# Kernel optimization log

Hardware: AMD Instinct MI355X
Metric: run time of the kernel (lower is better)

## Reference

```python
import jax, jax.numpy as jnp
import numpy as np

B, H, D, E = 64, 8, 64, 512          # batch, heads, head_dim, embed_dim
NB, BS = 32, 128                     # blocks per sequence, block size
L = NB * BS                          # max kv length (4096)
POS = 2048                           # decode position in cache


def setup_inputs() -> dict:
    key = jax.random.key(0)
    ks = jax.random.split(key, 12)
    s = E ** -0.5
    return {
        "hidden_states": jax.random.normal(ks[0], (B, 1, E), jnp.float32),
        "q_w": jax.random.normal(ks[1], (E, E), jnp.float32) * s,
        "q_b": jnp.zeros((E,), jnp.float32),
        "k_w": jax.random.normal(ks[2], (E, E), jnp.float32) * s,
        "k_b": jnp.zeros((E,), jnp.float32),
        "v_w": jax.random.normal(ks[3], (E, E), jnp.float32) * s,
        "v_b": jnp.zeros((E,), jnp.float32),
        "o_w": jax.random.normal(ks[4], (E, E), jnp.float32) * s,
        "o_b": jnp.zeros((E,), jnp.float32),
        "kcache": jax.random.normal(ks[5], (B, H, NB, BS, D), jnp.float32),
        "vcache": jax.random.normal(ks[6], (B, H, NB, BS, D), jnp.float32),
        "attention_mask": jnp.zeros((B, 1, 1, L), jnp.float32),  # additive mask
        "cache_position": POS,
        "block_tables": jax.random.randint(ks[7], (B, NB), 0, NB, jnp.int32),
    }


def reference(hidden_states, q_w, q_b, k_w, k_b, v_w, v_b, o_w, o_b,
              kcache, vcache, attention_mask, cache_position, block_tables):
    scaling = D ** -0.5
    # projections for the single decode token; q is pre-scaled (op gets scale=1.0)
    q = (hidden_states[:, 0] @ q_w.T + q_b).reshape(B, H, D) * scaling
    k_new = (hidden_states[:, 0] @ k_w.T + k_b).reshape(B, H, D)
    v_new = (hidden_states[:, 0] @ v_w.T + v_b).reshape(B, H, D)

    # gather physical blocks per sequence via block table -> [B, NB, H, BS, D]
    bidx = jnp.arange(B)[:, None]
    k_g = kcache[bidx, :, block_tables].transpose(0, 2, 1, 3, 4).reshape(B, H, L, D)
    v_g = vcache[bidx, :, block_tables].transpose(0, 2, 1, 3, 4).reshape(B, H, L, D)

    # write current token's k/v at cache_position (paged cache update)
    k_g = k_g.at[:, :, cache_position, :].set(k_new)
    v_g = v_g.at[:, :, cache_position, :].set(v_new)

    # add-softmax attention: scores = qk + mask
    scores = jnp.einsum('bhd,bhld->bhl', q, k_g) + attention_mask[:, :, 0, :]
    attn = jax.nn.softmax(scores, axis=-1)
    ctx = jnp.einsum('bhl,bhld->bhd', attn, v_g).reshape(B, 1, E)
    return ctx @ o_w.T + o_b
```

## Files before the change

### kernel.cpp

```cpp
#include <hip/hip_runtime.h>
#include <math.h>

#define BB 64
#define HH 8
#define Dh 64
#define EE 512
#define NBLK 32
#define BSZ 128
#define LL 4096

__global__ __launch_bounds__(512) void qkv_proj(
    const float* __restrict__ hidden,
    const float* __restrict__ q_w, const float* __restrict__ q_b,
    const float* __restrict__ k_w, const float* __restrict__ k_b,
    const float* __restrict__ v_w, const float* __restrict__ v_b,
    float* __restrict__ ws)
{
    const int b = blockIdx.x;
    const int proj = blockIdx.y;
    const int e = threadIdx.x;
    __shared__ float sh[EE];
    sh[e] = hidden[b * EE + e];
    __syncthreads();

    const float* w; const float* bias; float* out; float scale;
    if (proj == 0)      { w = q_w; bias = q_b; out = ws;             scale = 0.125f; }
    else if (proj == 1) { w = k_w; bias = k_b; out = ws + BB * EE;   scale = 1.0f; }
    else                { w = v_w; bias = v_b; out = ws + 2*BB*EE;   scale = 1.0f; }

    const float4* wr = (const float4*)(w + (size_t)e * EE);
    const float4* h4 = (const float4*)sh;
    float acc = bias[e];
    #pragma unroll 8
    for (int i = 0; i < EE/4; ++i) {
        float4 a = wr[i]; float4 x = h4[i];
        acc += a.x*x.x + a.y*x.y + a.z*x.z + a.w*x.w;
    }
    out[b * EE + e] = acc * scale;
}

__global__ __launch_bounds__(512) void attn(
    const float* __restrict__ ws,
    const float* __restrict__ kcache, const float* __restrict__ vcache,
    const float* __restrict__ mask,
    const int* __restrict__ cpos_p,
    const int* __restrict__ btab,
    float* __restrict__ ctx)
{
    const int bh = blockIdx.x;
    const int b  = bh >> 3;
    const int tid = threadIdx.x;
    const int grp = tid >> 4;
    const int l16 = tid & 15;
    const int wave = tid >> 6;
    const int lane = tid & 63;

    __shared__ float  s_scores[LL];
    __shared__ float  s_q[Dh];
    __shared__ int    s_bt[NBLK];
    __shared__ float  s_red[8];
    __shared__ float  s_b;
    __shared__ float4 s_vp[8][16];

    const float* qv   = ws;
    const float* knew = ws + BB * EE;
    const float* vnew = ws + 2 * BB * EE;

    if (tid < Dh)   s_q[tid]  = qv[(size_t)bh * Dh + tid];
    if (tid < NBLK) s_bt[tid] = btab[b * NBLK + tid];
    const int cpos = *cpos_p;
    __syncthreads();

    const float4 q4 = ((const float4*)s_q)[l16];
    const size_t base = (size_t)bh * NBLK * BSZ * Dh;
    const float4* knew4 = (const float4*)(knew + (size_t)bh * Dh);
    const float4* vnew4 = (const float4*)(vnew + (size_t)bh * Dh);

    #pragma unroll 4
    for (int step = 0; step < LL/32; ++step) {
        const int row = step * 32 + grp;
        const int nb = row >> 7, j = row & (BSZ - 1);
        const float4* kr = (const float4*)(kcache + base + ((size_t)s_bt[nb] * BSZ + j) * Dh);
        if (row == cpos) kr = knew4;
        float4 kv = kr[l16];
        float p = q4.x*kv.x + q4.y*kv.y + q4.z*kv.z + q4.w*kv.w;
        p += __shfl_xor(p, 1); p += __shfl_xor(p, 2);
        p += __shfl_xor(p, 4); p += __shfl_xor(p, 8);
        if (l16 == 0) s_scores[row] = p;
    }
    __syncthreads();

    float loc[8];
    float m = -3.4e38f;
    const float* mrow = mask + (size_t)b * LL;
    #pragma unroll
    for (int i = 0; i < 8; ++i) {
        const int idx = tid + 512 * i;
        loc[i] = s_scores[idx] + mrow[idx];
        m = fmaxf(m, loc[i]);
    }
    #pragma unroll
    for (int o = 1; o < 64; o <<= 1) m = fmaxf(m, __shfl_xor(m, o));
    if (lane == 0) s_red[wave] = m;
    __syncthreads();
    if (tid == 0) {
        float mm = s_red[0];
        #pragma unroll
        for (int i = 1; i < 8; ++i) mm = fmaxf(mm, s_red[i]);
        s_b = mm;
    }
    __syncthreads();
    m = s_b;

    float ssum = 0.f;
    #pragma unroll
    for (int i = 0; i < 8; ++i) { loc[i] = expf(loc[i] - m); ssum += loc[i]; }
    #pragma unroll
    for (int o = 1; o < 64; o <<= 1) ssum += __shfl_xor(ssum, o);
    __syncthreads();
    if (lane == 0) s_red[wave] = ssum;
    __syncthreads();
    if (tid == 0) {
        float s = 0.f;
        #pragma unroll
        for (int i = 0; i < 8; ++i) s += s_red[i];
        s_b = 1.0f / s;
    }
    __syncthreads();
    const float inv = s_b;
    #pragma unroll
    for (int i = 0; i < 8; ++i) s_scores[tid + 512 * i] = loc[i] * inv;
    __syncthreads();

    float4 acc = make_float4(0.f, 0.f, 0.f, 0.f);
    #pragma unroll 4
    for (int step = 0; step < LL/32; ++step) {
        const int row = step * 32 + grp;
        const int nb = row >> 7, j = row & (BSZ - 1);
        const float4* vr = (const float4*)(vcache + base + ((size_t)s_bt[nb] * BSZ + j) * Dh);
        if (row == cpos) vr = vnew4;
        float4 vv = vr[l16];
        const float w = s_scores[row];
        acc.x += w * vv.x; acc.y += w * vv.y; acc.z += w * vv.z; acc.w += w * vv.w;
    }
    #pragma unroll
    for (int o = 16; o < 64; o <<= 1) {
        acc.x += __shfl_xor(acc.x, o);
        acc.y += __shfl_xor(acc.y, o);
        acc.z += __shfl_xor(acc.z, o);
        acc.w += __shfl_xor(acc.w, o);
    }
    if (lane < 16) s_vp[wave][l16] = acc;
    __syncthreads();
    if (tid < 16) {
        float4 t = s_vp[0][tid];
        #pragma unroll
        for (int w = 1; w < 8; ++w) {
            float4 u = s_vp[w][tid];
            t.x += u.x; t.y += u.y; t.z += u.z; t.w += u.w;
        }
        ((float4*)(ctx + (size_t)bh * Dh))[tid] = t;
    }
}

__global__ __launch_bounds__(512) void out_proj(
    const float* __restrict__ ctx,
    const float* __restrict__ o_w, const float* __restrict__ o_b,
    float* __restrict__ out)
{
    const int b = blockIdx.x;
    const int e = threadIdx.x;
    __shared__ float sh[EE];
    sh[e] = ctx[b * EE + e];
    __syncthreads();
    const float4* wr = (const float4*)(o_w + (size_t)e * EE);
    const float4* h4 = (const float4*)sh;
    float acc = o_b[e];
    #pragma unroll 8
    for (int i = 0; i < EE/4; ++i) {
        float4 a = wr[i]; float4 x = h4[i];
        acc += a.x*x.x + a.y*x.y + a.z*x.z + a.w*x.w;
    }
    out[b * EE + e] = acc;
}

extern "C" void kernel_launch(void* const* d_in, const int* in_sizes, int n_in,
                              void* d_out, int out_size, void* d_ws, size_t ws_size,
                              hipStream_t stream)
{
    const float* hidden = (const float*)d_in[0];
    const float* q_w = (const float*)d_in[1];
    const float* q_b = (const float*)d_in[2];
    const float* k_w = (const float*)d_in[3];
    const float* k_b = (const float*)d_in[4];
    const float* v_w = (const float*)d_in[5];
    const float* v_b = (const float*)d_in[6];
    const float* o_w = (const float*)d_in[7];
    const float* o_b = (const float*)d_in[8];
    const float* kcache = (const float*)d_in[9];
    const float* vcache = (const float*)d_in[10];
    const float* mask = (const float*)d_in[11];
    const int* cpos = (const int*)d_in[12];
    const int* btab = (const int*)d_in[13];

    float* ws  = (float*)d_ws;
    float* ctx = ws + 3 * BB * EE;

    qkv_proj<<<dim3(BB, 3), 512, 0, stream>>>(hidden, q_w, q_b, k_w, k_b, v_w, v_b, ws);
    attn<<<dim3(BB * HH), 512, 0, stream>>>(ws, kcache, vcache, mask, cpos, btab, ctx);
    out_proj<<<dim3(BB), 512, 0, stream>>>(ctx, o_w, o_b, (float*)d_out);
}
```

Baseline: 231.4 us.

## Fuse attention into single-pass online softmax and batch-tile projection GEMVs

The attention kernel now streams K and V together in one pass with an online softmax per 16-lane group, merging the 32 group partials at the end. This removes the 16KB score buffer, the separate max/sum/normalize phases and their barriers, and the second read sweep over the block table. Projection kernels now process 4 batch rows per block and split the output dimension and reduction across threads, so each weight load is reused across batch rows. Loads use nontemporal hints and fast __expf. The online rescaling adds per-row exp work, and the extra grid dimensions change occupancy.

```diff
diff --git a/kernel.cpp b/kernel.cpp
--- a/kernel.cpp
+++ b/kernel.cpp
@@ -8,6 +8,10 @@
 #define NBLK 32
 #define BSZ 128
 #define LL 4096
+#define BG 4
+#define RC 128
+
+typedef float f4 __attribute__((ext_vector_type(4)));
 
 __global__ __launch_bounds__(512) void qkv_proj(
     const float* __restrict__ hidden,
@@ -16,11 +20,16 @@
     const float* __restrict__ v_w, const float* __restrict__ v_b,
     float* __restrict__ ws)
 {
-    const int b = blockIdx.x;
-    const int proj = blockIdx.y;
-    const int e = threadIdx.x;
-    __shared__ float sh[EE];
-    sh[e] = hidden[b * EE + e];
+    const int bg = blockIdx.x, proj = blockIdx.y, chunk = blockIdx.z;
+    const int tid = threadIdx.x;
+    const int r  = tid & (RC - 1);
+    const int l4 = tid >> 7;
+
+    __shared__ float sh[BG][EE];
+    __shared__ float sp[4][BG][RC];
+
+    for (int i = tid; i < BG * EE; i += 512)
+        sh[i >> 9][i & (EE - 1)] = hidden[(bg * BG + (i >> 9)) * EE + (i & (EE - 1))];
     __syncthreads();
 
     const float* w; const float* bias; float* out; float scale;
@@ -28,15 +37,26 @@
     else if (proj == 1) { w = k_w; bias = k_b; out = ws + BB * EE;   scale = 1.0f; }
     else                { w = v_w; bias = v_b; out = ws + 2*BB*EE;   scale = 1.0f; }
 
-    const float4* wr = (const float4*)(w + (size_t)e * EE);
-    const float4* h4 = (const float4*)sh;
-    float acc = bias[e];
+    const int e = chunk * RC + r;
+    const float4* wr = (const float4*)(w + (size_t)e * EE + l4 * 128);
+    float acc[BG] = {0.f, 0.f, 0.f, 0.f};
     #pragma unroll 8
-    for (int i = 0; i < EE/4; ++i) {
-        float4 a = wr[i]; float4 x = h4[i];
-        acc += a.x*x.x + a.y*x.y + a.z*x.z + a.w*x.w;
-    }
-    out[b * EE + e] = acc * scale;
+    for (int i = 0; i < 32; ++i) {
+        const float4 a = wr[i];
+        #pragma unroll
+        for (int b = 0; b < BG; ++b) {
+            const float4 x = ((const float4*)sh[b])[l4 * 32 + i];
+            acc[b] += a.x*x.x + a.y*x.y + a.z*x.z + a.w*x.w;
+        }
+    }
+    #pragma unroll
+    for (int b = 0; b < BG; ++b) sp[l4][b][r] = acc[b];
+    __syncthreads();
+
+    const int b2 = tid >> 7, r2 = tid & (RC - 1);
+    const int e2 = chunk * RC + r2;
+    const float v = sp[0][b2][r2] + sp[1][b2][r2] + sp[2][b2][r2] + sp[3][b2][r2];
+    out[(bg * BG + b2) * EE + e2] = (v + bias[e2]) * scale;
 }
 
 __global__ __launch_bounds__(512) void attn(
@@ -52,15 +72,12 @@
     const int tid = threadIdx.x;
     const int grp = tid >> 4;
     const int l16 = tid & 15;
-    const int wave = tid >> 6;
-    const int lane = tid & 63;
-
-    __shared__ float  s_scores[LL];
+
     __shared__ float  s_q[Dh];
     __shared__ int    s_bt[NBLK];
-    __shared__ float  s_red[8];
-    __shared__ float  s_b;
-    __shared__ float4 s_vp[8][16];
+    __shared__ float  s_m[32];
+    __shared__ float  s_s[32];
+    __shared__ float4 s_acc[32][16];
 
     const float* qv   = ws;
     const float* knew = ws + BB * EE;
@@ -73,92 +90,71 @@
 
     const float4 q4 = ((const float4*)s_q)[l16];
     const size_t base = (size_t)bh * NBLK * BSZ * Dh;
-    const float4* knew4 = (const float4*)(knew + (size_t)bh * Dh);
-    const float4* vnew4 = (const float4*)(vnew + (size_t)bh * Dh);
-
-    #pragma unroll 4
-    for (int step = 0; step < LL/32; ++step) {
-        const int row = step * 32 + grp;
-        const int nb = row >> 7, j = row & (BSZ - 1);
-        const float4* kr = (const float4*)(kcache + base + ((size_t)s_bt[nb] * BSZ + j) * Dh);
-        if (row == cpos) kr = knew4;
-        float4 kv = kr[l16];
-        float p = q4.x*kv.x + q4.y*kv.y + q4.z*kv.z + q4.w*kv.w;
-        p += __shfl_xor(p, 1); p += __shfl_xor(p, 2);
-        p += __shfl_xor(p, 4); p += __shfl_xor(p, 8);
-        if (l16 == 0) s_scores[row] = p;
-    }
-    __syncthreads();
-
-    float loc[8];
-    float m = -3.4e38f;
+    const f4* knew4 = (const f4*)(knew + (size_t)bh * Dh);
+    const f4* vnew4 = (const f4*)(vnew + (size_t)bh * Dh);
     const float* mrow = mask + (size_t)b * LL;
-    #pragma unroll
-    for (int i = 0; i < 8; ++i) {
-        const int idx = tid + 512 * i;
-        loc[i] = s_scores[idx] + mrow[idx];
-        m = fmaxf(m, loc[i]);
-    }
-    #pragma unroll
-    for (int o = 1; o < 64; o <<= 1) m = fmaxf(m, __shfl_xor(m, o));
-    if (lane == 0) s_red[wave] = m;
-    __syncthreads();
-    if (tid == 0) {
-        float mm = s_red[0];
-        #pragma unroll
-        for (int i = 1; i < 8; ++i) mm = fmaxf(mm, s_red[i]);
-        s_b = mm;
-    }
-    __syncthreads();
-    m = s_b;
-
-    float ssum = 0.f;
-    #pragma unroll
-    for (int i = 0; i < 8; ++i) { loc[i] = expf(loc[i] - m); ssum += loc[i]; }
-    #pragma unroll
-    for (int o = 1; o < 64; o <<= 1) ssum += __shfl_xor(ssum, o);
-    __syncthreads();
-    if (lane == 0) s_red[wave] = ssum;
-    __syncthreads();
-    if (tid == 0) {
-        float s = 0.f;
-        #pragma unroll
-        for (int i = 0; i < 8; ++i) s += s_red[i];
-        s_b = 1.0f / s;
-    }
-    __syncthreads();
-    const float inv = s_b;
-    #pragma unroll
-    for (int i = 0; i < 8; ++i) s_scores[tid + 512 * i] = loc[i] * inv;
-    __syncthreads();
-
+
+    float m = -3.4e38f, s = 0.f;
     float4 acc = make_float4(0.f, 0.f, 0.f, 0.f);
-    #pragma unroll 4
-    for (int step = 0; step < LL/32; ++step) {
-        const int row = step * 32 + grp;
-        const int nb = row >> 7, j = row & (BSZ - 1);
-        const float4* vr = (const float4*)(vcache + base + ((size_t)s_bt[nb] * BSZ + j) * Dh);
-        if (row == cpos) vr = vnew4;
-        float4 vv = vr[l16];
-        const float w = s_scores[row];
-        acc.x += w * vv.x; acc.y += w * vv.y; acc.z += w * vv.z; acc.w += w * vv.w;
-    }
-    #pragma unroll
-    for (int o = 16; o < 64; o <<= 1) {
-        acc.x += __shfl_xor(acc.x, o);
-        acc.y += __shfl_xor(acc.y, o);
-        acc.z += __shfl_xor(acc.z, o);
-        acc.w += __shfl_xor(acc.w, o);
-    }
-    if (lane < 16) s_vp[wave][l16] = acc;
-    __syncthreads();
+
+    #pragma unroll 2
+    for (int c = 0; c < NBLK; ++c) {
+        const size_t pb = base + (size_t)s_bt[c] * (BSZ * Dh);
+        #pragma unroll
+        for (int s4 = 0; s4 < 4; ++s4) {
+            const int rl  = s4 * 32 + grp;
+            const int row = c * BSZ + rl;
+            const f4* kr = (const f4*)(kcache + pb + (size_t)rl * Dh);
+            const f4* vr = (const f4*)(vcache + pb + (size_t)rl * Dh);
+            if (row == cpos) { kr = knew4; vr = vnew4; }
+            const f4 kv = __builtin_nontemporal_load(kr + l16);
+            const f4 vv = __builtin_nontemporal_load(vr + l16);
+
+            float p = q4.x*kv.x + q4.y*kv.y + q4.z*kv.z + q4.w*kv.w;
+            p += __shfl_xor(p, 1); p += __shfl_xor(p, 2);
+            p += __shfl_xor(p, 4); p += __shfl_xor(p, 8);
+            p += mrow[row];
+
+            const float mn = fmaxf(m, p);
+            const float cr = __expf(m - mn);
+            const float wt = __expf(p - mn);
+            s = s * cr + wt;
+            acc.x = acc.x * cr + wt * vv.x;
+            acc.y = acc.y * cr + wt * vv.y;
+            acc.z = acc.z * cr + wt * vv.z;
+            acc.w = acc.w * cr + wt * vv.w;
+            m = mn;
+        }
+    }
+
+    if (l16 == 0) { s_m[grp] = m; s_s[grp] = s; }
+    s_acc[grp][l16] = acc;
+    __syncthreads();
+
+    if (tid < 32) {
+        const float mg = s_m[tid];
+        float M = mg;
+        #pragma unroll
+        for (int o = 1; o < 32; o <<= 1) M = fmaxf(M, __shfl_xor(M, o));
+        const float c = __expf(mg - M);
+        float st = s_s[tid] * c;
+        #pragma unroll
+        for (int o = 1; o < 32; o <<= 1) st += __shfl_xor(st, o);
+        s_m[tid] = c;
+        if (tid == 0) s_s[0] = 1.0f / st;
+    }
+    __syncthreads();
+
     if (tid < 16) {
-        float4 t = s_vp[0][tid];
-        #pragma unroll
-        for (int w = 1; w < 8; ++w) {
-            float4 u = s_vp[w][tid];
-            t.x += u.x; t.y += u.y; t.z += u.z; t.w += u.w;
-        }
+        const float inv = s_s[0];
+        float4 t = make_float4(0.f, 0.f, 0.f, 0.f);
+        #pragma unroll
+        for (int g = 0; g < 32; ++g) {
+            const float c = s_m[g];
+            const float4 u = s_acc[g][tid];
+            t.x += c * u.x; t.y += c * u.y; t.z += c * u.z; t.w += c * u.w;
+        }
+        t.x *= inv; t.y *= inv; t.z *= inv; t.w *= inv;
         ((float4*)(ctx + (size_t)bh * Dh))[tid] = t;
     }
 }
@@ -168,20 +164,38 @@
     const float* __restrict__ o_w, const float* __restrict__ o_b,
     float* __restrict__ out)
 {
-    const int b = blockIdx.x;
-    const int e = threadIdx.x;
-    __shared__ float sh[EE];
-    sh[e] = ctx[b * EE + e];
-    __syncthreads();
-    const float4* wr = (const float4*)(o_w + (size_t)e * EE);
-    const float4* h4 = (const float4*)sh;
-    float acc = o_b[e];
+    const int bg = blockIdx.x, chunk = blockIdx.y;
+    const int tid = threadIdx.x;
+    const int r  = tid & (RC - 1);
+    const int l4 = tid >> 7;
+
+    __shared__ float sh[BG][EE];
+    __shared__ float sp[4][BG][RC];
+
+    for (int i = tid; i < BG * EE; i += 512)
+        sh[i >> 9][i & (EE - 1)] = ctx[(bg * BG + (i >> 9)) * EE + (i & (EE - 1))];
+    __syncthreads();
+
+    const int e = chunk * RC + r;
+    const float4* wr = (const float4*)(o_w + (size_t)e * EE + l4 * 128);
+    float acc[BG] = {0.f, 0.f, 0.f, 0.f};
     #pragma unroll 8
-    for (int i = 0; i < EE/4; ++i) {
-        float4 a = wr[i]; float4 x = h4[i];
-        acc += a.x*x.x + a.y*x.y + a.z*x.z + a.w*x.w;
-    }
-    out[b * EE + e] = acc;
+    for (int i = 0; i < 32; ++i) {
+        const float4 a = wr[i];
+        #pragma unroll
+        for (int b = 0; b < BG; ++b) {
+            const float4 x = ((const float4*)sh[b])[l4 * 32 + i];
+            acc[b] += a.x*x.x + a.y*x.y + a.z*x.z + a.w*x.w;
+        }
+    }
+    #pragma unroll
+    for (int b = 0; b < BG; ++b) sp[l4][b][r] = acc[b];
+    __syncthreads();
+
+    const int b2 = tid >> 7, r2 = tid & (RC - 1);
+    const int e2 = chunk * RC + r2;
+    const float v = sp[0][b2][r2] + sp[1][b2][r2] + sp[2][b2][r2] + sp[3][b2][r2];
+    out[(bg * BG + b2) * EE + e2] = v + o_b[e2];
 }
 
 extern "C" void kernel_launch(void* const* d_in, const int* in_sizes, int n_in,
@@ -206,7 +220,7 @@
     float* ws  = (float*)d_ws;
     float* ctx = ws + 3 * BB * EE;
 
-    qkv_proj<<<dim3(BB, 3), 512, 0, stream>>>(hidden, q_w, q_b, k_w, k_b, v_w, v_b, ws);
+    qkv_proj<<<dim3(BB/BG, 3, EE/RC), 512, 0, stream>>>(hidden, q_w, q_b, k_w, k_b, v_w, v_b, ws);
     attn<<<dim3(BB * HH), 512, 0, stream>>>(ws, kcache, vcache, mask, cpos, btab, ctx);
-    out_proj<<<dim3(BB), 512, 0, stream>>>(ctx, o_w, o_b, (float*)d_out);
-}
+    out_proj<<<dim3(BB/BG, EE/RC), 512, 0, stream>>>(ctx, o_w, o_b, (float*)d_out);
+}
```

Result: faster. 191.1 us (-17.4%).
